# Kernel tuning notes

Hardware: AMD Instinct MI355X
Metric: run time of the kernel (lower is better)

Reference implementation:

```python
import jax, jax.numpy as jnp
import numpy as np

B, S, D_IN, D_OUT = 4, 2048, 1024, 1024

def setup_inputs() -> dict:
    key = jax.random.key(0)
    k_x, k_q, k_k, k_v = jax.random.split(key, 4)
    return {
        "x": jax.random.normal(k_x, (B, S, D_IN), dtype=jnp.float32),
        "W_query": jax.random.uniform(k_q, (D_IN, D_OUT), dtype=jnp.float32),
        "W_key": jax.random.uniform(k_k, (D_IN, D_OUT), dtype=jnp.float32),
        "W_value": jax.random.uniform(k_v, (D_IN, D_OUT), dtype=jnp.float32),
    }

def reference(x, W_query, W_key, W_value):
    seq_len = x.shape[1]
    d_out = W_key.shape[-1]
    # fused QKV projection: x @ concat([Wq, Wk, Wv], -1), then split
    qkv = x @ jnp.concatenate([W_query, W_key, W_value], axis=-1)  # [B,S,3*d_out]
    query, key, value = jnp.split(qkv, 3, axis=2)
    # raw scores [B,S,S]; causal mask applied BEFORE scaling (as in source)
    attn_weights = jnp.einsum("bqd,bkd->bqk", query, key)
    causal = jnp.triu(jnp.ones((seq_len, seq_len), dtype=bool), k=1)
    attn_weights = jnp.where(causal[None, :, :], -jnp.inf, attn_weights)
    scaled = attn_weights / jnp.asarray(d_out, x.dtype) ** 0.5
    attn_scores = jax.nn.softmax(scaled, axis=-1)  # dropout p=0 -> identity
    context_vectors = jnp.einsum("bqk,bkd->bqd", attn_scores, value)
    return (context_vectors, attn_scores)
```

## Files before the change

kernel.cpp:

```cpp
#include <hip/hip_runtime.h>
#include <cstdint>
#include <cstddef>


#define S_LEN 2048
#define D_DIM 1024
#define NBATCH 4
#define MEG (1024 * 1024)

typedef __attribute__((ext_vector_type(4))) float floatx4;
typedef __attribute__((ext_vector_type(8))) __bf16 bf16x8;
typedef __attribute__((ext_vector_type(8))) short short8v;

__device__ __forceinline__ unsigned short f2bf(float f) {
  union { float f; unsigned u; } v; v.f = f;
  unsigned r = v.u + 0x7FFF + ((v.u >> 16) & 1);
  return (unsigned short)(r >> 16);
}
__device__ __forceinline__ float bf2f(unsigned short h) {
  union { unsigned u; float f; } v; v.u = ((unsigned)h) << 16; return v.f;
}

__device__ __forceinline__ void async_copy16(const void* g, void* l) {
  __builtin_amdgcn_global_load_lds(
      (const __attribute__((address_space(1))) void*)g,
      (__attribute__((address_space(3))) void*)l, 16, 0, 0);
}


__device__ __forceinline__ void gemm_bt_core(
    const short* __restrict__ A, const short* __restrict__ B,
    int lda, int ldb, int kIters, int blockM, int blockN,
    short (*As)[32], short (*Bs)[32], floatx4 (&acc)[4][4])
{
  const int tid  = threadIdx.x;
  const int lane = tid & 63;
  const int wave = tid >> 6;
  const int wm = (wave >> 1) * 64;
  const int wn = (wave & 1) * 64;
  const int fm = lane & 15;
  const int fk = (lane >> 4) * 8;
  const int r0 = tid >> 2;
  const int c0 = (tid & 3) * 8;

  floatx4 zero = {0.f, 0.f, 0.f, 0.f};
  #pragma unroll
  for (int i = 0; i < 4; ++i)
    #pragma unroll
    for (int j = 0; j < 4; ++j)
      acc[i][j] = zero;

  const short* a0 = A + (size_t)(blockM + r0) * lda + c0;
  const short* a1 = a0 + (size_t)64 * lda;
  const short* b0 = B + (size_t)(blockN + r0) * ldb + c0;
  const short* b1 = b0 + (size_t)64 * ldb;
  short* as0 = &As[r0][c0];
  short* as1 = &As[r0 + 64][c0];
  short* bs0 = &Bs[r0][c0];
  short* bs1 = &Bs[r0 + 64][c0];

  for (int kt = 0; kt < kIters; ++kt) {
    const int kb = kt * 32;
    async_copy16(a0 + kb, as0);
    async_copy16(a1 + kb, as1);
    async_copy16(b0 + kb, bs0);
    async_copy16(b1 + kb, bs1);
    __syncthreads();
    bf16x8 af[4], bfr[4];
    #pragma unroll
    for (int i = 0; i < 4; ++i)
      af[i] = *(const bf16x8*)(&As[wm + i * 16 + fm][fk]);
    #pragma unroll
    for (int j = 0; j < 4; ++j)
      bfr[j] = *(const bf16x8*)(&Bs[wn + j * 16 + fm][fk]);
    #pragma unroll
    for (int i = 0; i < 4; ++i)
      #pragma unroll
      for (int j = 0; j < 4; ++j)
        acc[i][j] = __builtin_amdgcn_mfma_f32_16x16x32_bf16(af[i], bfr[j], acc[i][j], 0, 0, 0);
    __syncthreads();
  }
}

__device__ __forceinline__ void gemm_bt_split_core(
    const short* __restrict__ Ah, const short* __restrict__ Al,
    const short* __restrict__ Bh, const short* __restrict__ Bl,
    int lda, int ldb, int kIters, int blockM, int blockN,
    short (*AsH)[32], short (*AsL)[32], short (*BsH)[32], short (*BsL)[32],
    floatx4 (&acc)[4][4])
{
  const int tid  = threadIdx.x;
  const int lane = tid & 63;
  const int wave = tid >> 6;
  const int wm = (wave >> 1) * 64;
  const int wn = (wave & 1) * 64;
  const int fm = lane & 15;
  const int fk = (lane >> 4) * 8;
  const int r0 = tid >> 2;
  const int c0 = (tid & 3) * 8;

  floatx4 zero = {0.f, 0.f, 0.f, 0.f};
  #pragma unroll
  for (int i = 0; i < 4; ++i)
    #pragma unroll
    for (int j = 0; j < 4; ++j)
      acc[i][j] = zero;

  const size_t oa0 = (size_t)(blockM + r0) * lda + c0;
  const size_t oa1 = oa0 + (size_t)64 * lda;
  const size_t ob0 = (size_t)(blockN + r0) * ldb + c0;
  const size_t ob1 = ob0 + (size_t)64 * ldb;
  short* lah0 = &AsH[r0][c0]; short* lah1 = &AsH[r0 + 64][c0];
  short* lal0 = &AsL[r0][c0]; short* lal1 = &AsL[r0 + 64][c0];
  short* lbh0 = &BsH[r0][c0]; short* lbh1 = &BsH[r0 + 64][c0];
  short* lbl0 = &BsL[r0][c0]; short* lbl1 = &BsL[r0 + 64][c0];

  for (int kt = 0; kt < kIters; ++kt) {
    const int kb = kt * 32;
    async_copy16(Ah + oa0 + kb, lah0);
    async_copy16(Ah + oa1 + kb, lah1);
    async_copy16(Al + oa0 + kb, lal0);
    async_copy16(Al + oa1 + kb, lal1);
    async_copy16(Bh + ob0 + kb, lbh0);
    async_copy16(Bh + ob1 + kb, lbh1);
    async_copy16(Bl + ob0 + kb, lbl0);
    async_copy16(Bl + ob1 + kb, lbl1);
    __syncthreads();
    bf16x8 ah[4], al[4], bh[4], bl[4];
    #pragma unroll
    for (int i = 0; i < 4; ++i) {
      ah[i] = *(const bf16x8*)(&AsH[wm + i * 16 + fm][fk]);
      al[i] = *(const bf16x8*)(&AsL[wm + i * 16 + fm][fk]);
    }
    #pragma unroll
    for (int j = 0; j < 4; ++j) {
      bh[j] = *(const bf16x8*)(&BsH[wn + j * 16 + fm][fk]);
      bl[j] = *(const bf16x8*)(&BsL[wn + j * 16 + fm][fk]);
    }
    #pragma unroll
    for (int i = 0; i < 4; ++i)
      #pragma unroll
      for (int j = 0; j < 4; ++j) {
        acc[i][j] = __builtin_amdgcn_mfma_f32_16x16x32_bf16(ah[i], bh[j], acc[i][j], 0, 0, 0);
        acc[i][j] = __builtin_amdgcn_mfma_f32_16x16x32_bf16(ah[i], bl[j], acc[i][j], 0, 0, 0);
        acc[i][j] = __builtin_amdgcn_mfma_f32_16x16x32_bf16(al[i], bh[j], acc[i][j], 0, 0, 0);
      }
    __syncthreads();
  }
}


__global__ __launch_bounds__(256) void k_cvt(
    const float4* __restrict__ x,
    const float* __restrict__ wq, const float* __restrict__ wk,
    const float* __restrict__ wv,
    short* __restrict__ xh, short* __restrict__ xl,
    short* __restrict__ wqh, short* __restrict__ wql,
    short* __restrict__ wkh, short* __restrict__ wkl,
    short* __restrict__ wvt, float* __restrict__ muSum)
{
  const int bid = blockIdx.x;
  const int tid = threadIdx.x;
  if (bid < 5120) {
    const float4* src;
    short *dh, *dl;
    size_t idx;
    if (bid < 4096) {
      idx = (size_t)bid * 256 + tid;
      src = x; dh = xh; dl = xl;
    } else if (bid < 4608) {
      idx = (size_t)(bid - 4096) * 256 + tid;
      src = (const float4*)wq; dh = wqh; dl = wql;
    } else {
      idx = (size_t)(bid - 4608) * 256 + tid;
      src = (const float4*)wk; dh = wkh; dl = wkl;
    }
    const float4 u4 = src[idx * 2];
    const float4 w4 = src[idx * 2 + 1];
    float f[8] = {u4.x, u4.y, u4.z, u4.w, w4.x, w4.y, w4.z, w4.w};
    short8v oh, ol;
    #pragma unroll
    for (int e = 0; e < 8; ++e) {
      const unsigned short h = f2bf(f[e]);
      oh[e] = (short)h;
      ol[e] = (short)f2bf(f[e] - bf2f(h));
    }
    *(short8v*)(dh + idx * 8) = oh;
    *(short8v*)(dl + idx * 8) = ol;
  } else {
    if (bid == 5120) {
      float4 z = {0.f, 0.f, 0.f, 0.f};
      ((float4*)muSum)[tid] = z;
    }
    const int rem = bid - 5120;
    const int bx = rem & 31, by = rem >> 5;
    const int tx = tid & 31, ty = tid >> 5;
    __shared__ float tile[32][33];
    const int colIn = bx * 32 + tx;
    #pragma unroll
    for (int i = 0; i < 4; ++i) {
      const int rowIn = by * 32 + ty + i * 8;
      tile[ty + i * 8][tx] = wv[(size_t)rowIn * D_DIM + colIn];
    }
    __syncthreads();
    const int colOut = by * 32 + tx;
    #pragma unroll
    for (int i = 0; i < 4; ++i) {
      const int rowOut = bx * 32 + ty + i * 8;
      wvt[(size_t)rowOut * D_DIM + colOut] = (short)f2bf(tile[tx][ty + i * 8]);
    }
  }
}


__global__ __launch_bounds__(256) void k_gemm_m(
    const short* __restrict__ wqh, const short* __restrict__ wql,
    const short* __restrict__ wkh, const short* __restrict__ wkl,
    short* __restrict__ mth, short* __restrict__ mtl,
    float* __restrict__ muSum)
{
  __shared__ alignas(16) short AsH[128][32];
  __shared__ alignas(16) short AsL[128][32];
  __shared__ alignas(16) short BsH[128][32];
  __shared__ alignas(16) short BsL[128][32];
  floatx4 acc[4][4];
  const int blockM = blockIdx.y * 128;
  const int blockN = blockIdx.x * 128;
  gemm_bt_split_core(wkh, wkl, wqh, wql,
                     D_DIM, D_DIM, D_DIM / 32, blockM, blockN,
                     AsH, AsL, BsH, BsL, acc);

  const int tid = threadIdx.x, lane = tid & 63, wave = tid >> 6;
  const int wm = (wave >> 1) * 64, wn = (wave & 1) * 64;
  const int rb = wm + ((lane >> 4) << 2);
  const int cb = wn + (lane & 15);
  #pragma unroll
  for (int i = 0; i < 4; ++i)
    #pragma unroll
    for (int j = 0; j < 4; ++j) {
      const int n = blockN + cb + j * 16;
      #pragma unroll
      for (int r = 0; r < 4; ++r) {
        const int m = blockM + rb + i * 16 + r;
        const float f = acc[i][j][r];
        const unsigned short h = f2bf(f);
        mth[(size_t)m * D_DIM + n] = (short)h;
        mtl[(size_t)m * D_DIM + n] = (short)f2bf(f - bf2f(h));
      }
    }
  #pragma unroll
  for (int i = 0; i < 4; ++i)
    #pragma unroll
    for (int r = 0; r < 4; ++r) {
      float v = acc[i][0][r] + acc[i][1][r] + acc[i][2][r] + acc[i][3][r];
      v += __shfl_xor(v, 1); v += __shfl_xor(v, 2);
      v += __shfl_xor(v, 4); v += __shfl_xor(v, 8);
      if ((lane & 15) == 0)
        atomicAdd(&muSum[blockM + rb + i * 16 + r], v);
    }
}


__global__ __launch_bounds__(256) void k_rowstats(
    const short* __restrict__ xh, const short* __restrict__ xl,
    const float* __restrict__ muSum, float* __restrict__ sq, float* __restrict__ u)
{
  const int r = blockIdx.x, tid = threadIdx.x;
  const ushort4 h = *(const ushort4*)(xh + (size_t)r * D_DIM + tid * 4);
  const ushort4 l = *(const ushort4*)(xl + (size_t)r * D_DIM + tid * 4);
  const float4 m4 = *(const float4*)(muSum + tid * 4);
  const float x0 = bf2f(h.x) + bf2f(l.x);
  const float x1 = bf2f(h.y) + bf2f(l.y);
  const float x2 = bf2f(h.z) + bf2f(l.z);
  const float x3 = bf2f(h.w) + bf2f(l.w);
  float s = x0 + x1 + x2 + x3;
  float uu = m4.x * x0 + m4.y * x1 + m4.z * x2 + m4.w * x3;
  #pragma unroll
  for (int off = 32; off > 0; off >>= 1) {
    s  += __shfl_xor(s, off);
    uu += __shfl_xor(uu, off);
  }
  __shared__ float ps[4], pu[4];
  if ((tid & 63) == 0) { ps[tid >> 6] = s; pu[tid >> 6] = uu; }
  __syncthreads();
  if (tid == 0) {
    sq[r] = ps[0] + ps[1] + ps[2] + ps[3];
    u[r]  = (pu[0] + pu[1] + pu[2] + pu[3]) * (1.0f / 1024.0f);
  }
}


__global__ __launch_bounds__(256) void k_gemm_n(
    const short* __restrict__ xh, const short* __restrict__ xl,
    const short* __restrict__ mth, const short* __restrict__ mtl,
    const float* __restrict__ sq, const float* __restrict__ muSum,
    short* __restrict__ nh, short* __restrict__ nl)
{
  __shared__ alignas(16) short AsH[128][32];
  __shared__ alignas(16) short AsL[128][32];
  __shared__ alignas(16) short BsH[128][32];
  __shared__ alignas(16) short BsL[128][32];
  floatx4 acc[4][4];
  const int blockM = blockIdx.y * 128;
  const int blockN = blockIdx.x * 128;
  gemm_bt_split_core(xh, xl, mth, mtl, D_DIM, D_DIM, D_DIM / 32,
                     blockM, blockN, AsH, AsL, BsH, BsL, acc);

  const int tid = threadIdx.x, lane = tid & 63, wave = tid >> 6;
  const int wm = (wave >> 1) * 64, wn = (wave & 1) * 64;
  const int rb = wm + ((lane >> 4) << 2);
  const int cb = wn + (lane & 15);
  #pragma unroll
  for (int i = 0; i < 4; ++i)
    #pragma unroll
    for (int j = 0; j < 4; ++j) {
      const int n = blockN + cb + j * 16;
      const float muv = muSum[n] * (1.0f / 1024.0f);
      #pragma unroll
      for (int r = 0; r < 4; ++r) {
        const int m = blockM + rb + i * 16 + r;
        const float f = acc[i][j][r] - sq[m] * muv;
        const unsigned short h = f2bf(f);
        nh[(size_t)m * D_DIM + n] = (short)h;
        nl[(size_t)m * D_DIM + n] = (short)f2bf(f - bf2f(h));
      }
    }
}


__global__ __launch_bounds__(256) void k_gemm_v(
    const short* __restrict__ xh, const short* __restrict__ wvt,
    short* __restrict__ vt)
{
  __shared__ alignas(16) short As[128][32];
  __shared__ alignas(16) short Bs[128][32];
  floatx4 acc[4][4];
  const int blockM = blockIdx.y * 128;
  const int blockN = blockIdx.x * 128;
  gemm_bt_core(xh, wvt, D_DIM, D_DIM, D_DIM / 32, blockM, blockN, As, Bs, acc);

  const int tid = threadIdx.x, lane = tid & 63, wave = tid >> 6;
  const int wm = (wave >> 1) * 64, wn = (wave & 1) * 64;
  const int rb = wm + ((lane >> 4) << 2);
  const int cb = wn + (lane & 15);
  #pragma unroll
  for (int i = 0; i < 4; ++i)
    #pragma unroll
    for (int j = 0; j < 4; ++j) {
      const int n = blockN + cb + j * 16;
      const int m0 = blockM + rb + i * 16;
      const int b = m0 >> 11;
      const int s0 = m0 & (S_LEN - 1);
      ushort4 pk;
      pk.x = f2bf(acc[i][j][0]); pk.y = f2bf(acc[i][j][1]);
      pk.z = f2bf(acc[i][j][2]); pk.w = f2bf(acc[i][j][3]);
      *(ushort4*)(vt + ((size_t)b * D_DIM + n) * S_LEN + s0) = pk;
    }
}


__global__ __launch_bounds__(256) void k_gemm_s(
    const short* __restrict__ nh, const short* __restrict__ nl,
    const short* __restrict__ xh, const short* __restrict__ xl,
    const float* __restrict__ sq, const float* __restrict__ u,
    float* __restrict__ attn)
{
  __shared__ alignas(16) short AsH[128][32];
  __shared__ alignas(16) short AsL[128][32];
  __shared__ alignas(16) short BsH[128][32];
  __shared__ alignas(16) short BsL[128][32];
  floatx4 acc[4][4];

  const int g = blockIdx.x;
  const int item = (g & 7) * 68 + (g >> 3);
  const int b = item / 136;
  int t = item - b * 136;
  int band = 0;
  while (t >= 58 - 16 * band) { t -= 58 - 16 * band; ++band; }
  int bi = band * 4;
  for (;;) {
    const int w = bi - band * 4 + 1;
    const int ww = w < 4 ? w : 4;
    if (t < ww) break;
    t -= ww; ++bi;
  }
  const int bj = band * 4 + t;

  const size_t boff = (size_t)b * S_LEN * D_DIM;
  gemm_bt_split_core(nh + boff, nl + boff, xh + boff, xl + boff,
                     D_DIM, D_DIM, D_DIM / 32, bi * 128, bj * 128,
                     AsH, AsL, BsH, BsL, acc);

  float* out = attn + (size_t)b * S_LEN * S_LEN;
  const int tid = threadIdx.x, lane = tid & 63, wave = tid >> 6;
  const int wm = (wave >> 1) * 64, wn = (wave & 1) * 64;
  const int rb = wm + ((lane >> 4) << 2);
  const int cb = wn + (lane & 15);
  const int rowBase = (b << 11) + bi * 128;
  const int colBase = (b << 11) + bj * 128;
  #pragma unroll
  for (int j = 0; j < 4; ++j) {
    const int n = bj * 128 + cb + j * 16;
    const float uv = u[colBase + cb + j * 16];
    #pragma unroll
    for (int i = 0; i < 4; ++i)
      #pragma unroll
      for (int r = 0; r < 4; ++r) {
        const int m = bi * 128 + rb + i * 16 + r;
        const float sv = sq[rowBase + rb + i * 16 + r];
        out[(size_t)m * S_LEN + n] = acc[i][j][r] + sv * uv;
      }
  }
}


__global__ __launch_bounds__(256) void k_softmax(float* __restrict__ attn,
                                                 short* __restrict__ pb) {
  const int b = blockIdx.x >> 11;
  const int q = blockIdx.x & (S_LEN - 1);
  float* row  = attn + ((size_t)b * S_LEN + q) * S_LEN;
  short* prow = pb   + ((size_t)b * S_LEN + q) * S_LEN;
  const int tid = threadIdx.x;
  const int k0 = tid * 8;
  __shared__ float sMax[4], sSum[4];

  const float4 a0 = *(const float4*)(row + k0);
  const float4 a1 = *(const float4*)(row + k0 + 4);
  float v[8] = {a0.x, a0.y, a0.z, a0.w, a1.x, a1.y, a1.z, a1.w};

  float mx = -3.0e38f;
  #pragma unroll
  for (int e = 0; e < 8; ++e) {
    v[e] = (k0 + e <= q) ? v[e] : -3.0e38f;
    mx = fmaxf(mx, v[e]);
  }
  #pragma unroll
  for (int off = 32; off > 0; off >>= 1) mx = fmaxf(mx, __shfl_xor(mx, off));
  if ((tid & 63) == 0) sMax[tid >> 6] = mx;
  __syncthreads();
  mx = fmaxf(fmaxf(sMax[0], sMax[1]), fmaxf(sMax[2], sMax[3]));

  float s = 0.f;
  #pragma unroll
  for (int e = 0; e < 8; ++e) {
    const float p = (k0 + e <= q) ? __expf((v[e] - mx) * 0.03125f) : 0.f;
    v[e] = p;
    s += p;
  }
  #pragma unroll
  for (int off = 32; off > 0; off >>= 1) s += __shfl_xor(s, off);
  if ((tid & 63) == 0) sSum[tid >> 6] = s;
  __syncthreads();
  s = sSum[0] + sSum[1] + sSum[2] + sSum[3];
  const float inv = 1.0f / s;

  float o[8];
  #pragma unroll
  for (int e = 0; e < 8; ++e) o[e] = v[e] * inv;
  float4 w0 = {o[0], o[1], o[2], o[3]};
  float4 w1 = {o[4], o[5], o[6], o[7]};
  *(float4*)(row + k0) = w0;
  *(float4*)(row + k0 + 4) = w1;
  ushort4 p0, p1;
  p0.x = f2bf(o[0]); p0.y = f2bf(o[1]); p0.z = f2bf(o[2]); p0.w = f2bf(o[3]);
  p1.x = f2bf(o[4]); p1.y = f2bf(o[5]); p1.z = f2bf(o[6]); p1.w = f2bf(o[7]);
  *(ushort4*)(prow + k0) = p0;
  *(ushort4*)(prow + k0 + 4) = p1;
}


__global__ __launch_bounds__(256) void k_gemm_ctx(
    const short* __restrict__ pb, const short* __restrict__ vt,
    float* __restrict__ ctx)
{
  __shared__ alignas(16) short As[128][32];
  __shared__ alignas(16) short Bs[128][32];
  floatx4 acc[4][4];
  const int b = blockIdx.z;
  const int by = 15 - blockIdx.y;
  const int blockM = by * 128;
  const int blockN = blockIdx.x * 128;
  const int kIters = by * 4 + 4;
  const short* A = pb + (size_t)b * S_LEN * S_LEN;
  const short* B = vt + (size_t)b * D_DIM * S_LEN;
  gemm_bt_core(A, B, S_LEN, S_LEN, kIters, blockM, blockN, As, Bs, acc);

  float* out = ctx + (size_t)b * S_LEN * D_DIM;
  const int tid = threadIdx.x, lane = tid & 63, wave = tid >> 6;
  const int wm = (wave >> 1) * 64, wn = (wave & 1) * 64;
  const int rb = wm + ((lane >> 4) << 2);
  const int cb = wn + (lane & 15);
  #pragma unroll
  for (int i = 0; i < 4; ++i)
    #pragma unroll
    for (int j = 0; j < 4; ++j) {
      const int n = blockN + cb + j * 16;
      #pragma unroll
      for (int r = 0; r < 4; ++r) {
        const int m = blockM + rb + i * 16 + r;
        out[(size_t)m * D_DIM + n] = acc[i][j][r];
      }
    }
}


extern "C" void kernel_launch(void* const* d_in, const int* in_sizes, int n_in,
                              void* d_out, int out_size, void* d_ws, size_t ws_size,
                              hipStream_t stream) {
  const float* x  = (const float*)d_in[0];
  const float* wq = (const float*)d_in[1];
  const float* wk = (const float*)d_in[2];
  const float* wv = (const float*)d_in[3];

  float* out  = (float*)d_out;
  float* ctx  = out;
  float* attn = out + (size_t)NBATCH * S_LEN * D_DIM;

  short* ws  = (short*)d_ws;
  short* xh  = ws;
  short* xl  = xh + (size_t)8 * MEG;
  short* wqh = xl + (size_t)8 * MEG;
  short* wql = wqh + (size_t)1 * MEG;
  short* wkh = wql + (size_t)1 * MEG;
  short* wkl = wkh + (size_t)1 * MEG;
  short* wvt = wkl + (size_t)1 * MEG;
  short* mth = wvt + (size_t)1 * MEG;
  short* mtl = mth + (size_t)1 * MEG;
  short* nh  = mtl + (size_t)1 * MEG;
  short* nl  = nh + (size_t)8 * MEG;
  short* vt  = nl + (size_t)8 * MEG;
  short* pb  = nh;
  float* fb  = (float*)(vt + (size_t)8 * MEG);
  float* muS = fb;
  float* sq  = fb + 1024;
  float* u   = sq + 8192;

  k_cvt<<<6144, 256, 0, stream>>>((const float4*)x, wq, wk, wv,
                                  xh, xl, wqh, wql, wkh, wkl, wvt, muS);
  k_gemm_m<<<dim3(8, 8), 256, 0, stream>>>(wqh, wql, wkh, wkl, mth, mtl, muS);
  k_rowstats<<<8192, 256, 0, stream>>>(xh, xl, muS, sq, u);
  k_gemm_n<<<dim3(8, 64), 256, 0, stream>>>(xh, xl, mth, mtl, sq, muS, nh, nl);
  k_gemm_v<<<dim3(8, 64), 256, 0, stream>>>(xh, wvt, vt);
  k_gemm_s<<<544, 256, 0, stream>>>(nh, nl, xh, xl, sq, u, attn);
  k_softmax<<<NBATCH * S_LEN, 256, 0, stream>>>(attn, pb);
  k_gemm_ctx<<<dim3(8, 16, 4), 256, 0, stream>>>(pb, vt, ctx);
}
```

Baseline: 431.8 us.

## Merge V projection into score GEMM launch and skip masked softmax loads/stores

The V projection GEMM now runs inside the score GEMM as 512 extra blocks of one combined launch. The idea is that the two independent GEMMs share the machine and fill the tail of the triangular score workload. The softmax kernel no longer loads score values for fully masked 8-element chunks. It also writes bf16 probabilities only up to the 128-aligned causal band that the context GEMM actually reads. This cuts memory traffic, but relies on the ctx GEMM never reading pb beyond that band.

Measured after the change: 409.8 us. 1.05x faster.

```diff
diff --git a/kernel.cpp b/kernel.cpp
--- a/kernel.cpp
+++ b/kernel.cpp
@@ -328,42 +328,12 @@
 }
 
 
-__global__ __launch_bounds__(256) void k_gemm_v(
-    const short* __restrict__ xh, const short* __restrict__ wvt,
-    short* __restrict__ vt)
-{
-  __shared__ alignas(16) short As[128][32];
-  __shared__ alignas(16) short Bs[128][32];
-  floatx4 acc[4][4];
-  const int blockM = blockIdx.y * 128;
-  const int blockN = blockIdx.x * 128;
-  gemm_bt_core(xh, wvt, D_DIM, D_DIM, D_DIM / 32, blockM, blockN, As, Bs, acc);
-
-  const int tid = threadIdx.x, lane = tid & 63, wave = tid >> 6;
-  const int wm = (wave >> 1) * 64, wn = (wave & 1) * 64;
-  const int rb = wm + ((lane >> 4) << 2);
-  const int cb = wn + (lane & 15);
-  #pragma unroll
-  for (int i = 0; i < 4; ++i)
-    #pragma unroll
-    for (int j = 0; j < 4; ++j) {
-      const int n = blockN + cb + j * 16;
-      const int m0 = blockM + rb + i * 16;
-      const int b = m0 >> 11;
-      const int s0 = m0 & (S_LEN - 1);
-      ushort4 pk;
-      pk.x = f2bf(acc[i][j][0]); pk.y = f2bf(acc[i][j][1]);
-      pk.z = f2bf(acc[i][j][2]); pk.w = f2bf(acc[i][j][3]);
-      *(ushort4*)(vt + ((size_t)b * D_DIM + n) * S_LEN + s0) = pk;
-    }
-}
-
-
-__global__ __launch_bounds__(256) void k_gemm_s(
+__global__ __launch_bounds__(256) void k_gemm_sv(
     const short* __restrict__ nh, const short* __restrict__ nl,
     const short* __restrict__ xh, const short* __restrict__ xl,
     const float* __restrict__ sq, const float* __restrict__ u,
-    float* __restrict__ attn)
+    const short* __restrict__ wvt, float* __restrict__ attn,
+    short* __restrict__ vt)
 {
   __shared__ alignas(16) short AsH[128][32];
   __shared__ alignas(16) short AsL[128][32];
@@ -372,43 +342,65 @@
   floatx4 acc[4][4];
 
   const int g = blockIdx.x;
-  const int item = (g & 7) * 68 + (g >> 3);
-  const int b = item / 136;
-  int t = item - b * 136;
-  int band = 0;
-  while (t >= 58 - 16 * band) { t -= 58 - 16 * band; ++band; }
-  int bi = band * 4;
-  for (;;) {
-    const int w = bi - band * 4 + 1;
-    const int ww = w < 4 ? w : 4;
-    if (t < ww) break;
-    t -= ww; ++bi;
-  }
-  const int bj = band * 4 + t;
-
-  const size_t boff = (size_t)b * S_LEN * D_DIM;
-  gemm_bt_split_core(nh + boff, nl + boff, xh + boff, xl + boff,
-                     D_DIM, D_DIM, D_DIM / 32, bi * 128, bj * 128,
-                     AsH, AsL, BsH, BsL, acc);
-
-  float* out = attn + (size_t)b * S_LEN * S_LEN;
   const int tid = threadIdx.x, lane = tid & 63, wave = tid >> 6;
   const int wm = (wave >> 1) * 64, wn = (wave & 1) * 64;
   const int rb = wm + ((lane >> 4) << 2);
   const int cb = wn + (lane & 15);
-  const int rowBase = (b << 11) + bi * 128;
-  const int colBase = (b << 11) + bj * 128;
-  #pragma unroll
-  for (int j = 0; j < 4; ++j) {
-    const int n = bj * 128 + cb + j * 16;
-    const float uv = u[colBase + cb + j * 16];
+
+  if (g < 544) {
+    const int item = (g & 7) * 68 + (g >> 3);
+    const int b = item / 136;
+    int t = item - b * 136;
+    int band = 0;
+    while (t >= 58 - 16 * band) { t -= 58 - 16 * band; ++band; }
+    int bi = band * 4;
+    for (;;) {
+      const int w = bi - band * 4 + 1;
+      const int ww = w < 4 ? w : 4;
+      if (t < ww) break;
+      t -= ww; ++bi;
+    }
+    const int bj = band * 4 + t;
+
+    const size_t boff = (size_t)b * S_LEN * D_DIM;
+    gemm_bt_split_core(nh + boff, nl + boff, xh + boff, xl + boff,
+                       D_DIM, D_DIM, D_DIM / 32, bi * 128, bj * 128,
+                       AsH, AsL, BsH, BsL, acc);
+
+    float* out = attn + (size_t)b * S_LEN * S_LEN;
+    const int rowBase = (b << 11) + bi * 128;
+    const int colBase = (b << 11) + bj * 128;
+    #pragma unroll
+    for (int j = 0; j < 4; ++j) {
+      const int n = bj * 128 + cb + j * 16;
+      const float uv = u[colBase + cb + j * 16];
+      #pragma unroll
+      for (int i = 0; i < 4; ++i)
+        #pragma unroll
+        for (int r = 0; r < 4; ++r) {
+          const int m = bi * 128 + rb + i * 16 + r;
+          const float sv = sq[rowBase + rb + i * 16 + r];
+          out[(size_t)m * S_LEN + n] = acc[i][j][r] + sv * uv;
+        }
+    }
+  } else {
+    const int vb = g - 544;
+    const int blockM = (vb >> 3) * 128;
+    const int blockN = (vb & 7) * 128;
+    gemm_bt_core(xh, wvt, D_DIM, D_DIM, D_DIM / 32, blockM, blockN,
+                 AsH, BsH, acc);
     #pragma unroll
     for (int i = 0; i < 4; ++i)
       #pragma unroll
-      for (int r = 0; r < 4; ++r) {
-        const int m = bi * 128 + rb + i * 16 + r;
-        const float sv = sq[rowBase + rb + i * 16 + r];
-        out[(size_t)m * S_LEN + n] = acc[i][j][r] + sv * uv;
+      for (int j = 0; j < 4; ++j) {
+        const int n = blockN + cb + j * 16;
+        const int m0 = blockM + rb + i * 16;
+        const int b = m0 >> 11;
+        const int s0 = m0 & (S_LEN - 1);
+        ushort4 pk;
+        pk.x = f2bf(acc[i][j][0]); pk.y = f2bf(acc[i][j][1]);
+        pk.z = f2bf(acc[i][j][2]); pk.w = f2bf(acc[i][j][3]);
+        *(ushort4*)(vt + ((size_t)b * D_DIM + n) * S_LEN + s0) = pk;
       }
   }
 }
@@ -422,11 +414,19 @@
   short* prow = pb   + ((size_t)b * S_LEN + q) * S_LEN;
   const int tid = threadIdx.x;
   const int k0 = tid * 8;
+  const int kBand = ((q >> 7) + 1) << 7;
   __shared__ float sMax[4], sSum[4];
 
-  const float4 a0 = *(const float4*)(row + k0);
-  const float4 a1 = *(const float4*)(row + k0 + 4);
-  float v[8] = {a0.x, a0.y, a0.z, a0.w, a1.x, a1.y, a1.z, a1.w};
+  float v[8];
+  if (k0 <= q) {
+    const float4 a0 = *(const float4*)(row + k0);
+    const float4 a1 = *(const float4*)(row + k0 + 4);
+    v[0] = a0.x; v[1] = a0.y; v[2] = a0.z; v[3] = a0.w;
+    v[4] = a1.x; v[5] = a1.y; v[6] = a1.z; v[7] = a1.w;
+  } else {
+    #pragma unroll
+    for (int e = 0; e < 8; ++e) v[e] = -3.0e38f;
+  }
 
   float mx = -3.0e38f;
   #pragma unroll
@@ -461,11 +461,13 @@
   float4 w1 = {o[4], o[5], o[6], o[7]};
   *(float4*)(row + k0) = w0;
   *(float4*)(row + k0 + 4) = w1;
-  ushort4 p0, p1;
-  p0.x = f2bf(o[0]); p0.y = f2bf(o[1]); p0.z = f2bf(o[2]); p0.w = f2bf(o[3]);
-  p1.x = f2bf(o[4]); p1.y = f2bf(o[5]); p1.z = f2bf(o[6]); p1.w = f2bf(o[7]);
-  *(ushort4*)(prow + k0) = p0;
-  *(ushort4*)(prow + k0 + 4) = p1;
+  if (k0 < kBand) {
+    ushort4 p0, p1;
+    p0.x = f2bf(o[0]); p0.y = f2bf(o[1]); p0.z = f2bf(o[2]); p0.w = f2bf(o[3]);
+    p1.x = f2bf(o[4]); p1.y = f2bf(o[5]); p1.z = f2bf(o[6]); p1.w = f2bf(o[7]);
+    *(ushort4*)(prow + k0) = p0;
+    *(ushort4*)(prow + k0 + 4) = p1;
+  }
 }
 
 
@@ -540,8 +542,7 @@
   k_gemm_m<<<dim3(8, 8), 256, 0, stream>>>(wqh, wql, wkh, wkl, mth, mtl, muS);
   k_rowstats<<<8192, 256, 0, stream>>>(xh, xl, muS, sq, u);
   k_gemm_n<<<dim3(8, 64), 256, 0, stream>>>(xh, xl, mth, mtl, sq, muS, nh, nl);
-  k_gemm_v<<<dim3(8, 64), 256, 0, stream>>>(xh, wvt, vt);
-  k_gemm_s<<<544, 256, 0, stream>>>(nh, nl, xh, xl, sq, u, attn);
+  k_gemm_sv<<<1056, 256, 0, stream>>>(nh, nl, xh, xl, sq, u, wvt, attn, vt);
   k_softmax<<<NBATCH * S_LEN, 256, 0, stream>>>(attn, pb);
   k_gemm_ctx<<<dim3(8, 16, 4), 256, 0, stream>>>(pb, vt, ctx);
 }
```
